# Performance work log

Hardware: AMD Instinct MI355X
Metric: run time of the kernel (lower is better)

The kernel has to match this reference:

```python
import jax, jax.numpy as jnp
import numpy as np

B, S, D = 2, 1024, 1024
H, HD = 16, 64          # n_heads, head_dim (H*HD == D)
E, FF = 8, 2816         # num_experts, moe hidden_dim
TOP_K = 2               # hard-coded torch.topk(scores, 2)
EPS = 1e-5


def rmsnorm(x, w):
    return x * jax.lax.rsqrt(jnp.mean(x * x, axis=-1, keepdims=True) + EPS) * w


def apply_rope(x, cos, sin):
    # x: [B,S,H,HD]; cos/sin: [S,HD//2] -> interleaved rotary (llama style)
    xr, xi = x[..., 0::2], x[..., 1::2]
    c = cos[None, :, None, :]
    s = sin[None, :, None, :]
    out_r = xr * c - xi * s
    out_i = xr * s + xi * c
    return jnp.stack([out_r, out_i], axis=-1).reshape(x.shape)


def setup_inputs() -> dict:
    key = jax.random.key(0)
    ks = jax.random.split(key, 10)
    sc = 0.02
    pos = jnp.arange(S, dtype=jnp.float32)
    inv = 1.0 / (10000.0 ** (jnp.arange(0, HD, 2, dtype=jnp.float32) / HD))
    ang = pos[:, None] * inv[None, :]                       # [S, HD//2]
    return {
        "x": jax.random.normal(ks[0], (B, S, D), jnp.float32),
        "freqs_cos": jnp.cos(ang),
        "freqs_sin": jnp.sin(ang),
        "attn_norm_w": jnp.ones((D,), jnp.float32),
        "wq": jax.random.normal(ks[1], (D, D), jnp.float32) * sc,
        "wk": jax.random.normal(ks[2], (D, D), jnp.float32) * sc,
        "wv": jax.random.normal(ks[3], (D, D), jnp.float32) * sc,
        "wo": jax.random.normal(ks[4], (D, D), jnp.float32) * sc,
        "ffn_norm_w": jnp.ones((D,), jnp.float32),
        "gate_w": jax.random.normal(ks[5], (E, D), jnp.float32) * sc,
        "w1": jax.random.normal(ks[6], (E, FF, D), jnp.float32) * sc,
        "w2": jax.random.normal(ks[7], (E, FF, D), jnp.float32) * sc,
        "w3": jax.random.normal(ks[8], (E, FF, D), jnp.float32) * sc,
    }


def reference(x, freqs_cos, freqs_sin, attn_norm_w, wq, wk, wv, wo,
              ffn_norm_w, gate_w, w1, w2, w3):
    b, s, d = x.shape

    # ---- pre-norm attention + residual ----
    xn = rmsnorm(x, attn_norm_w)
    q = (xn @ wq.T).reshape(b, s, H, HD)
    k = (xn @ wk.T).reshape(b, s, H, HD)
    v = (xn @ wv.T).reshape(b, s, H, HD)
    q = apply_rope(q, freqs_cos, freqs_sin)
    k = apply_rope(k, freqs_cos, freqs_sin)
    scores = jnp.einsum("bqhd,bkhd->bhqk", q, k) / jnp.sqrt(jnp.float32(HD))
    causal = jnp.tril(jnp.ones((s, s), bool))
    scores = jnp.where(causal[None, None], scores, jnp.finfo(scores.dtype).min)
    attn = jax.nn.softmax(scores, axis=-1)
    o = jnp.einsum("bhqk,bkhd->bqhd", attn, v).reshape(b, s, d) @ wo.T
    h = x + o

    # ---- top-2 MoE FFN (math identical to gather-per-token einsums) ----
    t = rmsnorm(h, ffn_norm_w).reshape(-1, d)               # [T, D]
    T = t.shape[0]
    gate = t @ gate_w.T                                     # [T, E]
    expert_weights, expert_idx = jax.lax.top_k(gate, TOP_K)
    expert_weights = jax.nn.softmax(expert_weights, axis=-1)  # [T, 2]

    x1 = jax.nn.silu(jnp.einsum("td,efd->tef", t, w1))      # [T, E, FF]
    x3 = jnp.einsum("td,efd->tef", t, w3)                   # [T, E, FF]
    ta = jnp.arange(T)[:, None]
    g = x1[ta, expert_idx] * x3[ta, expert_idx]             # [T, 2, FF]
    gw = g * expert_weights[..., None]                      # fold routing weights
    h_full = jnp.zeros((T, E, FF), t.dtype).at[ta, expert_idx].add(gw)
    moe = jnp.einsum("tef,efd->td", h_full, w2)             # [T, D]

    return h + moe.reshape(b, s, d)
```

## Files before the change

kernel.cpp:

```cpp
#include <hip/hip_runtime.h>

#define DI __device__ __forceinline__

typedef __attribute__((ext_vector_type(8))) short short8;
typedef __attribute__((ext_vector_type(4))) float f32x4;

#define DM   1024
#define TT   2048
#define SEQ  1024
#define NHD  16
#define HDD  64
#define NE   8
#define FF   2816

DI ushort f2bf(float f){
  union { float f; unsigned u; } c; c.f = f;
  unsigned u = c.u;
  u += 0x7fffu + ((u >> 16) & 1u);
  return (ushort)(u >> 16);
}
DI float bf2f(ushort b){
  union { unsigned u; float f; } c; c.u = ((unsigned)b) << 16;
  return c.f;
}
DI unsigned pk2(float a, float b){ return (unsigned)f2bf(a) | ((unsigned)f2bf(b) << 16); }
DI uint2 mku2(unsigned a, unsigned b){ uint2 r; r.x = a; r.y = b; return r; }

DI f32x4 MFMA(short8 a, short8 b, f32x4 c){
  return __builtin_amdgcn_mfma_f32_16x16x32_bf16(a, b, c, 0, 0, 0);
}

DI void gload16(const void* g, void* l){
  __builtin_amdgcn_global_load_lds(
      (const __attribute__((address_space(1))) unsigned*)g,
      (__attribute__((address_space(3))) unsigned*)l, 16, 0, 0);
}

#define LDSWZB(row, p) (((row) * 128) + ((((p) ^ ((row) & 7))) * 16))

__global__ __launch_bounds__(256) void k_rmsnorm(const float* __restrict__ x,
                                                 const float* __restrict__ w,
                                                 ushort* __restrict__ xh,
                                                 ushort* __restrict__ xl)
{
  int row = blockIdx.x, tid = threadIdx.x;
  float4 v = ((const float4*)(x + (size_t)row * DM))[tid];
  float ss = v.x*v.x + v.y*v.y + v.z*v.z + v.w*v.w;
#pragma unroll
  for (int m = 32; m >= 1; m >>= 1) ss += __shfl_xor(ss, m);
  __shared__ float sh[4];
  if ((tid & 63) == 0) sh[tid >> 6] = ss;
  __syncthreads();
  ss = sh[0] + sh[1] + sh[2] + sh[3];
  float rstd = 1.0f / sqrtf(ss * (1.0f / DM) + 1e-5f);
  float4 wv = ((const float4*)w)[tid];
  float o0 = v.x * rstd * wv.x, o1 = v.y * rstd * wv.y;
  float o2 = v.z * rstd * wv.z, o3 = v.w * rstd * wv.w;
  ushort h0 = f2bf(o0), h1 = f2bf(o1), h2 = f2bf(o2), h3 = f2bf(o3);
  ((uint2*)(xh + (size_t)row * DM))[tid] =
      mku2((unsigned)h0 | ((unsigned)h1 << 16), (unsigned)h2 | ((unsigned)h3 << 16));
  ((uint2*)(xl + (size_t)row * DM))[tid] =
      mku2(pk2(o0 - bf2f(h0), o1 - bf2f(h1)), pk2(o2 - bf2f(h2), o3 - bf2f(h3)));
}

__global__ __launch_bounds__(256) void k_wsplit(
    const float* __restrict__ wq, const float* __restrict__ wk,
    const float* __restrict__ wv, const float* __restrict__ wo,
    ushort* __restrict__ qh, ushort* __restrict__ ql,
    ushort* __restrict__ kh, ushort* __restrict__ kl,
    ushort* __restrict__ vh, ushort* __restrict__ vl,
    ushort* __restrict__ oh, ushort* __restrict__ ol)
{
  int y = blockIdx.y;
  const float* W = y == 0 ? wq : (y == 1 ? wk : (y == 2 ? wv : wo));
  ushort* H = y == 0 ? qh : (y == 1 ? kh : (y == 2 ? vh : oh));
  ushort* L = y == 0 ? ql : (y == 1 ? kl : (y == 2 ? vl : ol));
  int i = blockIdx.x * 256 + threadIdx.x;
  float4 v = ((const float4*)W)[i];
  ushort h0 = f2bf(v.x), h1 = f2bf(v.y), h2 = f2bf(v.z), h3 = f2bf(v.w);
  ((uint2*)H)[i] = mku2((unsigned)h0 | ((unsigned)h1 << 16),
                        (unsigned)h2 | ((unsigned)h3 << 16));
  ((uint2*)L)[i] = mku2(pk2(v.x - bf2f(h0), v.y - bf2f(h1)),
                        pk2(v.z - bf2f(h2), v.w - bf2f(h3)));
}

__global__ __launch_bounds__(256) void k_cw13(const float* __restrict__ w1,
                                              const float* __restrict__ w3,
                                              ushort* __restrict__ w1b,
                                              ushort* __restrict__ w3b)
{
  const float* src = blockIdx.y ? w3 : w1;
  ushort* dst = blockIdx.y ? w3b : w1b;
  const size_t N4 = (size_t)NE * FF * DM / 4;
  for (size_t i = (size_t)blockIdx.x * 256 + threadIdx.x; i < N4;
       i += (size_t)gridDim.x * 256) {
    float4 v = ((const float4*)src)[i];
    ((uint2*)dst)[i] = mku2(pk2(v.x, v.y), pk2(v.z, v.w));
  }
}

__global__ __launch_bounds__(256, 2) void k_gemm_qkv(
    const ushort* __restrict__ xh, const ushort* __restrict__ xl,
    const ushort* __restrict__ wqh, const ushort* __restrict__ wql,
    const ushort* __restrict__ wkh, const ushort* __restrict__ wkl,
    const ushort* __restrict__ wvh, const ushort* __restrict__ wvl,
    float* __restrict__ qf, float* __restrict__ kf,
    ushort* __restrict__ vh, ushort* __restrict__ vl)
{
  __shared__ __align__(16) char lds[65536];
  char* Ah = lds;          char* Al = lds + 16384;
  char* Bh = lds + 32768;  char* Bl = lds + 49152;
  int bn = blockIdx.x, bm = blockIdx.y;
  int which = bn >> 3, bnn = bn & 7;
  const ushort* WH = which == 0 ? wqh : (which == 1 ? wkh : wvh);
  const ushort* WL = which == 0 ? wql : (which == 1 ? wkl : wvl);
  int tid = threadIdx.x, lane = tid & 63, w = tid >> 6, wr = w >> 1, wc = w & 1;
  int r0 = lane >> 3, pp = lane & 7;
  size_t asrc[4], bsrc[4]; int cdst[4];
#pragma unroll
  for (int i = 0; i < 4; i++) {
    int c = w * 4 + i;
    int row = c * 8 + r0;
    asrc[i] = (size_t)(bm * 128 + row) * DM + (pp ^ r0) * 8;
    bsrc[i] = (size_t)(bnn * 128 + row) * DM + (pp ^ r0) * 8;
    cdst[i] = c * 1024;
  }
  f32x4 acc[4][4] = {};
  for (int kb = 0; kb < DM; kb += 64) {
    __syncthreads();
#pragma unroll
    for (int i = 0; i < 4; i++) {
      gload16(xh + asrc[i] + kb, Ah + cdst[i]);
      gload16(xl + asrc[i] + kb, Al + cdst[i]);
      gload16(WH + bsrc[i] + kb, Bh + cdst[i]);
      gload16(WL + bsrc[i] + kb, Bl + cdst[i]);
    }
    __syncthreads();
#pragma unroll
    for (int kk = 0; kk < 2; kk++) {
      int j = kk * 4 + (lane >> 4);
      short8 ar[4], al[4];
#pragma unroll
      for (int mi = 0; mi < 4; mi++) {
        int row = wr * 64 + mi * 16 + (lane & 15);
        ar[mi] = *(const short8*)(Ah + LDSWZB(row, j));
        al[mi] = *(const short8*)(Al + LDSWZB(row, j));
      }
#pragma unroll
      for (int ni = 0; ni < 4; ni++) {
        int n = wc * 64 + ni * 16 + (lane & 15);
        short8 b_h = *(const short8*)(Bh + LDSWZB(n, j));
        short8 b_l = *(const short8*)(Bl + LDSWZB(n, j));
#pragma unroll
        for (int mi = 0; mi < 4; mi++) {
          acc[mi][ni] = MFMA(ar[mi], b_h, acc[mi][ni]);
          acc[mi][ni] = MFMA(al[mi], b_h, acc[mi][ni]);
          acc[mi][ni] = MFMA(ar[mi], b_l, acc[mi][ni]);
        }
      }
    }
  }
#pragma unroll
  for (int mi = 0; mi < 4; mi++)
#pragma unroll
    for (int ni = 0; ni < 4; ni++)
#pragma unroll
      for (int r = 0; r < 4; r++) {
        int rg = bm*128 + wr*64 + mi*16 + (lane >> 4)*4 + r;
        int cg = bnn*128 + wc*64 + ni*16 + (lane & 15);
        float v = acc[mi][ni][r];
        if (which == 0)      qf[(size_t)rg * DM + cg] = v;
        else if (which == 1) kf[(size_t)rg * DM + cg] = v;
        else {
          int b = rg >> 10, s = rg & 1023, hh = cg >> 6, hd = cg & 63;
          size_t o = ((size_t)((b*NHD + hh)*HDD + hd)) * SEQ + s;
          ushort hv = f2bf(v);
          vh[o] = hv; vl[o] = f2bf(v - bf2f(hv));
        }
      }
}

__global__ __launch_bounds__(256) void k_rope(
    const float* __restrict__ qf, const float* __restrict__ kf,
    const float* __restrict__ fc, const float* __restrict__ fs,
    ushort* __restrict__ qh, ushort* __restrict__ ql,
    ushort* __restrict__ kh, ushort* __restrict__ kl)
{
  int t = blockIdx.x, tid = threadIdx.x;
  int b = t >> 10, s = t & 1023;
#pragma unroll
  for (int i = 0; i < 2; i++) {
    int p = tid + i*256;
    int hh = p >> 5, pi = p & 31;
    float c = fc[s*32 + pi], sn = fs[s*32 + pi];
    size_t o = ((size_t)(b*NHD + hh) * SEQ + s) * HDD + pi*2;
    {
      float2 v = *(const float2*)(qf + (size_t)t * DM + hh*HDD + pi*2);
      float r0 = v.x*c - v.y*sn, r1 = v.x*sn + v.y*c;
      ushort a0 = f2bf(r0), a1 = f2bf(r1);
      *(unsigned*)(qh + o) = (unsigned)a0 | ((unsigned)a1 << 16);
      *(unsigned*)(ql + o) = pk2(r0 - bf2f(a0), r1 - bf2f(a1));
    }
    {
      float2 v = *(const float2*)(kf + (size_t)t * DM + hh*HDD + pi*2);
      float r0 = v.x*c - v.y*sn, r1 = v.x*sn + v.y*c;
      ushort a0 = f2bf(r0), a1 = f2bf(r1);
      *(unsigned*)(kh + o) = (unsigned)a0 | ((unsigned)a1 << 16);
      *(unsigned*)(kl + o) = pk2(r0 - bf2f(a0), r1 - bf2f(a1));
    }
  }
}

__global__ __launch_bounds__(256) void k_attn(
    const ushort* __restrict__ qh_, const ushort* __restrict__ ql_,
    const ushort* __restrict__ kh_, const ushort* __restrict__ kl_,
    const ushort* __restrict__ vh_, const ushort* __restrict__ vl_,
    ushort* __restrict__ oh_, ushort* __restrict__ ol_)
{
  __shared__ __align__(16) ushort Kh[64*64], Kl[64*64], Vh[64*64], Vl[64*64];
  __shared__ __align__(16) ushort Ph[4*16*64], Pl[4*16*64];
  int qt = blockIdx.x, bh = blockIdx.y;
  int tid = threadIdx.x, lane = tid & 63, w = tid >> 6;
  short8 qfh[2], qfl[2];
  int qrow = qt*64 + w*16 + (lane & 15);
#pragma unroll
  for (int ks = 0; ks < 2; ks++) {
    size_t g = ((size_t)bh * SEQ + qrow) * HDD + ks*32 + (lane >> 4)*8;
    qfh[ks] = *(const short8*)(qh_ + g);
    qfl[ks] = *(const short8*)(ql_ + g);
  }
  f32x4 oacc[4] = {};
  float mrun[4], lrun[4];
#pragma unroll
  for (int r = 0; r < 4; r++) { mrun[r] = -1e30f; lrun[r] = 0.0f; }

  for (int kt = 0; kt <= qt; kt++) {
    __syncthreads();
#pragma unroll
    for (int i = 0; i < 2; i++) {
      int c = tid + i*256, row = c >> 3, sl = c & 7;
      int d = row*64 + ((sl + row) & 7) * 8;
      size_t gk = ((size_t)bh * SEQ + kt*64 + row) * HDD + sl*8;
      *(uint4*)&Kh[d] = *(const uint4*)(kh_ + gk);
      *(uint4*)&Kl[d] = *(const uint4*)(kl_ + gk);
      size_t gv = ((size_t)bh * HDD + row) * SEQ + kt*64 + sl*8;
      *(uint4*)&Vh[d] = *(const uint4*)(vh_ + gv);
      *(uint4*)&Vl[d] = *(const uint4*)(vl_ + gv);
    }
    __syncthreads();
    f32x4 sa[4] = {};
#pragma unroll
    for (int j = 0; j < 4; j++) {
#pragma unroll
      for (int ks = 0; ks < 2; ks++) {
        int kr = j*16 + (lane & 15);
        int d = kr*64 + (((ks*4 + (lane >> 4)) + kr) & 7) * 8;
        short8 b_h = *(const short8*)&Kh[d];
        short8 b_l = *(const short8*)&Kl[d];
        sa[j] = MFMA(qfh[ks], b_h, sa[j]);
        sa[j] = MFMA(qfl[ks], b_h, sa[j]);
        sa[j] = MFMA(qfh[ks], b_l, sa[j]);
      }
    }
    float sv[4][4];
#pragma unroll
    for (int j = 0; j < 4; j++)
#pragma unroll
      for (int r = 0; r < 4; r++) {
        float xx = sa[j][r] * 0.125f;
        if (kt == qt) {
          int kv = j*16 + (lane & 15), qi = w*16 + (lane >> 4)*4 + r;
          if (kv > qi) xx = -1e30f;
        }
        sv[j][r] = xx;
      }
#pragma unroll
    for (int r = 0; r < 4; r++) {
      float mx = fmaxf(fmaxf(sv[0][r], sv[1][r]), fmaxf(sv[2][r], sv[3][r]));
#pragma unroll
      for (int m = 8; m >= 1; m >>= 1) mx = fmaxf(mx, __shfl_xor(mx, m));
      float mn = fmaxf(mrun[r], mx);
      float alp = __expf(mrun[r] - mn);
      mrun[r] = mn;
      float rs = 0.0f;
#pragma unroll
      for (int j = 0; j < 4; j++) { float pv = __expf(sv[j][r] - mn); sv[j][r] = pv; rs += pv; }
#pragma unroll
      for (int m = 8; m >= 1; m >>= 1) rs += __shfl_xor(rs, m);
      lrun[r] = lrun[r] * alp + rs;
#pragma unroll
      for (int hf = 0; hf < 4; hf++) oacc[hf][r] *= alp;
    }
#pragma unroll
    for (int j = 0; j < 4; j++)
#pragma unroll
      for (int r = 0; r < 4; r++) {
        int row = (lane >> 4)*4 + r, col = j*16 + (lane & 15);
        int d = w*1024 + row*64 + (((col >> 3) ^ (row & 7)) * 8) + (col & 7);
        ushort hv = f2bf(sv[j][r]);
        Ph[d] = hv; Pl[d] = f2bf(sv[j][r] - bf2f(hv));
      }
#pragma unroll
    for (int hf = 0; hf < 4; hf++) {
#pragma unroll
      for (int ks = 0; ks < 2; ks++) {
        int prow = lane & 15;
        int pg = ((ks*4 + (lane >> 4)) ^ (prow & 7)) * 8;
        short8 pfh = *(const short8*)&Ph[w*1024 + prow*64 + pg];
        short8 pfl = *(const short8*)&Pl[w*1024 + prow*64 + pg];
        int vrow = hf*16 + (lane & 15);
        int vd = vrow*64 + (((ks*4 + (lane >> 4)) + vrow) & 7) * 8;
        short8 vfh = *(const short8*)&Vh[vd];
        short8 vfl = *(const short8*)&Vl[vd];
        oacc[hf] = MFMA(pfh, vfh, oacc[hf]);
        oacc[hf] = MFMA(pfl, vfh, oacc[hf]);
        oacc[hf] = MFMA(pfh, vfl, oacc[hf]);
      }
    }
  }
  int b = bh >> 4, h = bh & 15;
#pragma unroll
  for (int r = 0; r < 4; r++) {
    float li = 1.0f / lrun[r];
    int srow = qt*64 + w*16 + (lane >> 4)*4 + r;
#pragma unroll
    for (int hf = 0; hf < 4; hf++) {
      float v = oacc[hf][r] * li;
      size_t o = ((size_t)(b*SEQ + srow)) * DM + h*HDD + hf*16 + (lane & 15);
      ushort hv = f2bf(v);
      oh_[o] = hv; ol_[o] = f2bf(v - bf2f(hv));
    }
  }
}

__global__ __launch_bounds__(256, 2) void k_gemm_wo(
    const ushort* __restrict__ oh, const ushort* __restrict__ ol,
    const ushort* __restrict__ woh, const ushort* __restrict__ wol,
    const float* __restrict__ x, float* __restrict__ hb)
{
  __shared__ __align__(16) char lds[49152];
  char* Ah = lds;          char* Al = lds + 8192;
  char* Bh = lds + 16384;  char* Bl = lds + 32768;
  int bnn = blockIdx.x, bm = blockIdx.y;
  int tid = threadIdx.x, lane = tid & 63, w = tid >> 6;
  int r0 = lane >> 3, pp = lane & 7;
  size_t asrc[2]; int adst[2];
#pragma unroll
  for (int i = 0; i < 2; i++) {
    int c = w * 2 + i;
    int row = c * 8 + r0;
    asrc[i] = (size_t)(bm * 64 + row) * DM + (pp ^ r0) * 8;
    adst[i] = c * 1024;
  }
  size_t bsrc[4]; int bdst[4];
#pragma unroll
  for (int i = 0; i < 4; i++) {
    int c = w * 4 + i;
    int row = c * 8 + r0;
    bsrc[i] = (size_t)(bnn * 128 + row) * DM + (pp ^ r0) * 8;
    bdst[i] = c * 1024;
  }
  f32x4 acc[4][2] = {};
  for (int kb = 0; kb < DM; kb += 64) {
    __syncthreads();
#pragma unroll
    for (int i = 0; i < 2; i++) {
      gload16(oh + asrc[i] + kb, Ah + adst[i]);
      gload16(ol + asrc[i] + kb, Al + adst[i]);
    }
#pragma unroll
    for (int i = 0; i < 4; i++) {
      gload16(woh + bsrc[i] + kb, Bh + bdst[i]);
      gload16(wol + bsrc[i] + kb, Bl + bdst[i]);
    }
    __syncthreads();
#pragma unroll
    for (int kk = 0; kk < 2; kk++) {
      int j = kk * 4 + (lane >> 4);
      short8 ar[4], al[4];
#pragma unroll
      for (int mi = 0; mi < 4; mi++) {
        int row = mi * 16 + (lane & 15);
        ar[mi] = *(const short8*)(Ah + LDSWZB(row, j));
        al[mi] = *(const short8*)(Al + LDSWZB(row, j));
      }
#pragma unroll
      for (int ni = 0; ni < 2; ni++) {
        int n = w * 32 + ni * 16 + (lane & 15);
        short8 b_h = *(const short8*)(Bh + LDSWZB(n, j));
        short8 b_l = *(const short8*)(Bl + LDSWZB(n, j));
#pragma unroll
        for (int mi = 0; mi < 4; mi++) {
          acc[mi][ni] = MFMA(ar[mi], b_h, acc[mi][ni]);
          acc[mi][ni] = MFMA(al[mi], b_h, acc[mi][ni]);
          acc[mi][ni] = MFMA(ar[mi], b_l, acc[mi][ni]);
        }
      }
    }
  }
#pragma unroll
  for (int mi = 0; mi < 4; mi++)
#pragma unroll
    for (int ni = 0; ni < 2; ni++)
#pragma unroll
      for (int r = 0; r < 4; r++) {
        int rg = bm*64 + mi*16 + (lane >> 4)*4 + r;
        int cg = bnn*128 + w*32 + ni*16 + (lane & 15);
        hb[(size_t)rg * DM + cg] = x[(size_t)rg * DM + cg] + acc[mi][ni][r];
      }
}

__global__ __launch_bounds__(256) void k_gate(
    const float* __restrict__ hb, const float* __restrict__ fw, const float* __restrict__ gwt,
    ushort* __restrict__ tb, int* __restrict__ idx, float* __restrict__ ew, int* __restrict__ cnt)
{
  int t = blockIdx.x, tid = threadIdx.x;
  float4 v = ((const float4*)(hb + (size_t)t * DM))[tid];
  float ss = v.x*v.x + v.y*v.y + v.z*v.z + v.w*v.w;
#pragma unroll
  for (int m = 32; m >= 1; m >>= 1) ss += __shfl_xor(ss, m);
  __shared__ float sh[4];
  if ((tid & 63) == 0) sh[tid >> 6] = ss;
  __syncthreads();
  ss = sh[0] + sh[1] + sh[2] + sh[3];
  float rstd = 1.0f / sqrtf(ss * (1.0f / DM) + 1e-5f);
  float4 wv = ((const float4*)fw)[tid];
  float tv0 = v.x*rstd*wv.x, tv1 = v.y*rstd*wv.y, tv2 = v.z*rstd*wv.z, tv3 = v.w*rstd*wv.w;
  ((uint2*)(tb + (size_t)t * DM))[tid] = mku2(pk2(tv0, tv1), pk2(tv2, tv3));
  float ge[8];
#pragma unroll
  for (int e = 0; e < 8; e++) {
    float4 gv = ((const float4*)(gwt + (size_t)e * DM))[tid];
    float s = tv0*gv.x + tv1*gv.y + tv2*gv.z + tv3*gv.w;
#pragma unroll
    for (int m = 32; m >= 1; m >>= 1) s += __shfl_xor(s, m);
    ge[e] = s;
  }
  __shared__ float gsh[4][8];
  if ((tid & 63) == 0) {
#pragma unroll
    for (int e = 0; e < 8; e++) gsh[tid >> 6][e] = ge[e];
  }
  __syncthreads();
  if (tid == 0) {
    float lg[8];
#pragma unroll
    for (int e = 0; e < 8; e++) lg[e] = gsh[0][e] + gsh[1][e] + gsh[2][e] + gsh[3][e];
    int i0 = 0;
    for (int e = 1; e < 8; e++) if (lg[e] > lg[i0]) i0 = e;
    int i1 = (i0 == 0) ? 1 : 0;
    for (int e = 0; e < 8; e++) if (e != i0 && lg[e] > lg[i1]) i1 = e;
    float ex = __expf(lg[i1] - lg[i0]);
    idx[2*t] = i0; idx[2*t+1] = i1;
    ew[2*t] = 1.0f / (1.0f + ex); ew[2*t+1] = ex / (1.0f + ex);
    atomicAdd(&cnt[i0], 1); atomicAdd(&cnt[i1], 1);
  }
}

__global__ void k_offsets(const int* __restrict__ cnt, int* __restrict__ off,
                          int* __restrict__ fil, int* __restrict__ tmap)
{
  if (threadIdx.x == 0 && blockIdx.x == 0) {
    int a = 0, nt = 0;
    for (int e = 0; e < 8; e++) {
      off[e] = a; a += cnt[e]; fil[e] = 0;
      int m = (cnt[e] + 127) >> 7;
      for (int j = 0; j < m; j++) { tmap[1 + nt] = (e << 8) | j; nt++; }
    }
    tmap[0] = nt;
  }
}

__global__ __launch_bounds__(256) void k_scatter(
    const int* __restrict__ idx, const int* __restrict__ off,
    int* __restrict__ fil, int* __restrict__ ent, int* __restrict__ pos)
{
  int t = blockIdx.x * 256 + threadIdx.x;
  if (t < TT) {
#pragma unroll
    for (int k = 0; k < 2; k++) {
      int e = idx[2*t + k];
      int p = atomicAdd(&fil[e], 1);
      int g = off[e] + p;
      ent[g] = 2*t + k;
      pos[2*t + k] = g;
    }
  }
}

__global__ __launch_bounds__(256) void k_tw2(const float* __restrict__ w2, ushort* __restrict__ w2t)
{
  int dt = blockIdx.x, ft = blockIdx.y, e = blockIdx.z;
  __shared__ ushort lt[64*72];
  int tid = threadIdx.x;
#pragma unroll
  for (int i = 0; i < 4; i++) {
    int c = tid + i*256;
    int r = c >> 4, q = c & 15;
    float4 v = *(const float4*)(w2 + ((size_t)e*FF + ft*64 + r) * DM + dt*64 + q*4);
    lt[(q*4+0)*72 + r] = f2bf(v.x);
    lt[(q*4+1)*72 + r] = f2bf(v.y);
    lt[(q*4+2)*72 + r] = f2bf(v.z);
    lt[(q*4+3)*72 + r] = f2bf(v.w);
  }
  __syncthreads();
#pragma unroll
  for (int i = 0; i < 2; i++) {
    int c = tid + i*256;
    int d = c >> 3, fq = c & 7;
    *(uint4*)(w2t + ((size_t)e*DM + dt*64 + d) * FF + ft*64 + fq*8) = *(const uint4*)&lt[d*72 + fq*8];
  }
}

__global__ __launch_bounds__(256, 4) void k_moe13(
    const ushort* __restrict__ tb, const ushort* __restrict__ w1b, const ushort* __restrict__ w3b,
    const int* __restrict__ ent, const float* __restrict__ ew,
    const int* __restrict__ cnt, const int* __restrict__ off, const int* __restrict__ tmap,
    ushort* __restrict__ gb)
{
  int y = blockIdx.y;
  if (y >= tmap[0]) return;
  int tm = tmap[1 + y];
  int e = tm >> 8, mt = tm & 255;
  int nt = blockIdx.x;
  int cn = cnt[e], oe = off[e];
  __shared__ __align__(16) char lds[32768];
  char* Ab = lds;
  char* B1 = lds + 16384;
  char* B3 = lds + 24576;
  int tid = threadIdx.x, lane = tid & 63, w = tid >> 6;
  int wr = w >> 1, wc = w & 1;
  int r0 = lane >> 3, pp = lane & 7;

  const ushort* abase = tb + (pp ^ r0) * 8;
  unsigned aoff[4];
#pragma unroll
  for (int i = 0; i < 4; i++) {
    int c = w * 4 + i;
    int r = c * 8 + r0;
    int g = oe + mt * 128 + r; if (g > 2*TT - 1) g = 2*TT - 1;
    aoff[i] = (unsigned)((ent[g] >> 1) * DM);
  }
  size_t bofs[2];
#pragma unroll
  for (int i = 0; i < 2; i++) {
    int c = 2 * w + i;
    bofs[i] = ((size_t)e * FF + nt * 64 + c * 8 + r0) * DM + (pp ^ r0) * 8;
  }

  f32x4 acc1[4][2] = {}, acc3[4][2] = {};

  for (int kb = 0; kb < DM; kb += 64) {
    __syncthreads();
#pragma unroll
    for (int i = 0; i < 4; i++)
      gload16(abase + aoff[i] + kb, Ab + (w * 4 + i) * 1024);
#pragma unroll
    for (int i = 0; i < 2; i++) {
      gload16(w1b + bofs[i] + kb, B1 + (2 * w + i) * 1024);
      gload16(w3b + bofs[i] + kb, B3 + (2 * w + i) * 1024);
    }
    __syncthreads();
#pragma unroll
    for (int kk = 0; kk < 2; kk++) {
      int j = kk * 4 + (lane >> 4);
      short8 af[4];
#pragma unroll
      for (int mi = 0; mi < 4; mi++) {
        int row = wr * 64 + mi * 16 + (lane & 15);
        af[mi] = *(const short8*)(Ab + LDSWZB(row, j));
      }
#pragma unroll
      for (int ni = 0; ni < 2; ni++) {
        int n = wc * 32 + ni * 16 + (lane & 15);
        short8 b1f = *(const short8*)(B1 + LDSWZB(n, j));
        short8 b3f = *(const short8*)(B3 + LDSWZB(n, j));
#pragma unroll
        for (int mi = 0; mi < 4; mi++) {
          acc1[mi][ni] = MFMA(af[mi], b1f, acc1[mi][ni]);
          acc3[mi][ni] = MFMA(af[mi], b3f, acc3[mi][ni]);
        }
      }
    }
  }
#pragma unroll
  for (int mi = 0; mi < 4; mi++)
#pragma unroll
    for (int ni = 0; ni < 2; ni++)
#pragma unroll
      for (int r = 0; r < 4; r++) {
        int grow = mt * 128 + wr * 64 + mi * 16 + (lane >> 4) * 4 + r;
        if (grow < cn) {
          int g = oe + grow;
          float gwv = ew[ent[g]];
          int f = nt * 64 + wc * 32 + ni * 16 + (lane & 15);
          float x1 = acc1[mi][ni][r], x3 = acc3[mi][ni][r];
          float sg = x1 / (1.0f + __expf(-x1));
          gb[(size_t)g * FF + f] = f2bf(sg * x3 * gwv);
        }
      }
}

__global__ __launch_bounds__(256, 4) void k_moe2(
    const ushort* __restrict__ gb, const ushort* __restrict__ w2t,
    const int* __restrict__ cnt, const int* __restrict__ off, const int* __restrict__ tmap,
    float* __restrict__ mr)
{
  int y = blockIdx.y;
  if (y >= tmap[0]) return;
  int tm = tmap[1 + y];
  int e = tm >> 8, mt = tm & 255;
  int nt = blockIdx.x;
  int cn = cnt[e], oe = off[e];
  __shared__ __align__(16) char lds[24576];
  char* Ab = lds; char* Bb = lds + 16384;
  int tid = threadIdx.x, lane = tid & 63, w = tid >> 6;
  int r0 = lane >> 3, pp = lane & 7;

  const ushort* abase = gb + (pp ^ r0) * 8;
  unsigned aoff[4];
#pragma unroll
  for (int i = 0; i < 4; i++) {
    int c = w * 4 + i;
    int r = c * 8 + r0;
    int g = oe + mt * 128 + r; if (g > 2*TT - 1) g = 2*TT - 1;
    aoff[i] = (unsigned)(g * FF);
  }
  size_t bofs[2];
#pragma unroll
  for (int i = 0; i < 2; i++) {
    int c = 2 * w + i;
    bofs[i] = ((size_t)e * DM + nt * 64 + c * 8 + r0) * FF + (pp ^ r0) * 8;
  }

  f32x4 acc[4][1] = {};
  f32x4 a2[2][4] = {};
  (void)acc;
  for (int kb = 0; kb < FF; kb += 64) {
    __syncthreads();
#pragma unroll
    for (int i = 0; i < 4; i++)
      gload16(abase + aoff[i] + kb, Ab + (w * 4 + i) * 1024);
#pragma unroll
    for (int i = 0; i < 2; i++)
      gload16(w2t + bofs[i] + kb, Bb + (2 * w + i) * 1024);
    __syncthreads();
#pragma unroll
    for (int kk = 0; kk < 2; kk++) {
      int j = kk * 4 + (lane >> 4);
      short8 af[2], bf[4];
#pragma unroll
      for (int mi = 0; mi < 2; mi++) {
        int row = w * 32 + mi * 16 + (lane & 15);
        af[mi] = *(const short8*)(Ab + LDSWZB(row, j));
      }
#pragma unroll
      for (int ni = 0; ni < 4; ni++) {
        int n = ni * 16 + (lane & 15);
        bf[ni] = *(const short8*)(Bb + LDSWZB(n, j));
      }
#pragma unroll
      for (int ni = 0; ni < 4; ni++)
#pragma unroll
        for (int mi = 0; mi < 2; mi++)
          a2[mi][ni] = MFMA(af[mi], bf[ni], a2[mi][ni]);
    }
  }
#pragma unroll
  for (int mi = 0; mi < 2; mi++)
#pragma unroll
    for (int ni = 0; ni < 4; ni++)
#pragma unroll
      for (int r = 0; r < 4; r++) {
        int grow = mt * 128 + w * 32 + mi * 16 + (lane >> 4) * 4 + r;
        if (grow < cn) {
          int cg = nt * 64 + ni * 16 + (lane & 15);
          mr[(size_t)(oe + grow) * DM + cg] = a2[mi][ni][r];
        }
      }
}

__global__ __launch_bounds__(256) void k_final(
    const float* __restrict__ hb, const float* __restrict__ mr,
    const int* __restrict__ pos, float* __restrict__ out)
{
  int t = blockIdx.x, tid = threadIdx.x;
  int g0 = pos[2*t], g1 = pos[2*t+1];
  float4 a  = ((const float4*)(hb + (size_t)t * DM))[tid];
  float4 m0 = ((const float4*)(mr + (size_t)g0 * DM))[tid];
  float4 m1 = ((const float4*)(mr + (size_t)g1 * DM))[tid];
  float4 o;
  o.x = a.x + m0.x + m1.x; o.y = a.y + m0.y + m1.y;
  o.z = a.z + m0.z + m1.z; o.w = a.w + m0.w + m1.w;
  ((float4*)(out + (size_t)t * DM))[tid] = o;
}

extern "C" void kernel_launch(void* const* d_in, const int* in_sizes, int n_in,
                              void* d_out, int out_size, void* d_ws, size_t ws_size,
                              hipStream_t stream)
{
  const float* x   = (const float*)d_in[0];
  const float* fc  = (const float*)d_in[1];
  const float* fs  = (const float*)d_in[2];
  const float* anw = (const float*)d_in[3];
  const float* wq  = (const float*)d_in[4];
  const float* wk  = (const float*)d_in[5];
  const float* wv  = (const float*)d_in[6];
  const float* wo  = (const float*)d_in[7];
  const float* fnw = (const float*)d_in[8];
  const float* gwm = (const float*)d_in[9];
  const float* w1  = (const float*)d_in[10];
  const float* w2  = (const float*)d_in[11];
  const float* w3  = (const float*)d_in[12];
  float* out = (float*)d_out;

  char* p = (char*)d_ws;
  auto alloc = [&](size_t n) { char* r = p; p += (n + 255) & ~(size_t)255; return r; };
  ushort* xnh = (ushort*)alloc((size_t)TT*DM*2);
  ushort* xnl = (ushort*)alloc((size_t)TT*DM*2);
  float*  qf  = (float*) alloc((size_t)TT*DM*4);
  float*  kf  = (float*) alloc((size_t)TT*DM*4);
  ushort* qh  = (ushort*)alloc((size_t)TT*DM*2);
  ushort* ql  = (ushort*)alloc((size_t)TT*DM*2);
  ushort* kh  = (ushort*)alloc((size_t)TT*DM*2);
  ushort* kl  = (ushort*)alloc((size_t)TT*DM*2);
  ushort* vh  = (ushort*)alloc((size_t)TT*DM*2);
  ushort* vl  = (ushort*)alloc((size_t)TT*DM*2);
  ushort* oh  = (ushort*)alloc((size_t)TT*DM*2);
  ushort* ol  = (ushort*)alloc((size_t)TT*DM*2);
  float*  hb  = (float*) alloc((size_t)TT*DM*4);
  ushort* tb  = (ushort*)alloc((size_t)TT*DM*2);
  ushort* w2t = (ushort*)alloc((size_t)NE*FF*DM*2);
  ushort* gb  = (ushort*)alloc((size_t)2*TT*FF*2);
  float*  mr  = (float*) alloc((size_t)2*TT*DM*4);
  int*    idx = (int*)   alloc((size_t)2*TT*4);
  float*  ew  = (float*) alloc((size_t)2*TT*4);
  int*    ent = (int*)   alloc((size_t)2*TT*4);
  int*    pos = (int*)   alloc((size_t)2*TT*4);
  int*    cnt = (int*)   alloc(32);
  int*    off = (int*)   alloc(32);
  int*    fil = (int*)   alloc(32);
  int*    tmap= (int*)   alloc(256);

  ushort* wsp = (ushort*)mr;
  const size_t WN = (size_t)DM * DM;
  ushort* wqh = wsp;        ushort* wql = wsp + WN;
  ushort* wkh = wsp + 2*WN; ushort* wkl = wsp + 3*WN;
  ushort* wvh = wsp + 4*WN; ushort* wvl = wsp + 5*WN;
  ushort* woh = wsp + 6*WN; ushort* wol = wsp + 7*WN;

  ushort* w1b = (ushort*)d_ws;
  ushort* w3b = (ushort*)alloc((size_t)NE*FF*DM*2);

  hipMemsetAsync(cnt, 0, 32, stream);
  k_rmsnorm<<<TT, 256, 0, stream>>>(x, anw, xnh, xnl);
  k_wsplit<<<dim3(1024, 4), 256, 0, stream>>>(wq, wk, wv, wo,
      wqh, wql, wkh, wkl, wvh, wvl, woh, wol);
  k_tw2<<<dim3(16, 44, 8), 256, 0, stream>>>(w2, w2t);
  k_gemm_qkv<<<dim3(24, 16), 256, 0, stream>>>(xnh, xnl,
      wqh, wql, wkh, wkl, wvh, wvl, qf, kf, vh, vl);
  k_rope<<<TT, 256, 0, stream>>>(qf, kf, fc, fs, qh, ql, kh, kl);
  k_attn<<<dim3(16, 32), 256, 0, stream>>>(qh, ql, kh, kl, vh, vl, oh, ol);
  k_gemm_wo<<<dim3(8, 32), 256, 0, stream>>>(oh, ol, woh, wol, x, hb);
  k_gate<<<TT, 256, 0, stream>>>(hb, fnw, gwm, tb, idx, ew, cnt);
  k_offsets<<<1, 64, 0, stream>>>(cnt, off, fil, tmap);
  k_scatter<<<8, 256, 0, stream>>>(idx, off, fil, ent, pos);
  k_cw13<<<dim3(2048, 2), 256, 0, stream>>>(w1, w3, w1b, w3b);
  k_moe13<<<dim3(44, 48), 256, 0, stream>>>(tb, w1b, w3b, ent, ew, cnt, off, tmap, gb);
  k_moe2<<<dim3(16, 48), 256, 0, stream>>>(gb, w2t, cnt, off, tmap, mr);
  k_final<<<TT, 256, 0, stream>>>(hb, mr, pos, out);
  (void)in_sizes; (void)n_in; (void)out_size; (void)ws_size;
}
```

Baseline: 458.5 us.

## Fuse fp32-to-bf16 conversion of w1/w3 into MoE up-projection GEMM

Drops the separate kernel that converted the full w1 and w3 expert weights to bf16. The k_moe13 GEMM now loads fp32 weight tiles into registers one k-step ahead, packs them to bf16 and stores them into swizzled LDS, with manual waitcnt and barriers so the next tile's load overlaps the current MFMA work. This removes a full write and re-read of the converted weights. In exchange each block reads fp32 weights, which is twice the bytes, and several token tiles per expert re-read them, so it also uses more registers (occupancy hint lowered from 4 to 3).

```diff
diff --git a/kernel.cpp b/kernel.cpp
--- a/kernel.cpp
+++ b/kernel.cpp
@@ -37,6 +37,11 @@
 }
 
 #define LDSWZB(row, p) (((row) * 128) + ((((p) ^ ((row) & 7))) * 16))
+
+#define VMCNT(N) asm volatile("s_waitcnt vmcnt(" #N ")" ::: "memory")
+#define LGKM0()  asm volatile("s_waitcnt lgkmcnt(0)" ::: "memory")
+#define SBAR()   __builtin_amdgcn_s_barrier()
+#define SCHED0() __builtin_amdgcn_sched_barrier(0)
 
 __global__ __launch_bounds__(256) void k_rmsnorm(const float* __restrict__ x,
                                                  const float* __restrict__ w,
@@ -84,21 +89,6 @@
                         pk2(v.z - bf2f(h2), v.w - bf2f(h3)));
 }
 
-__global__ __launch_bounds__(256) void k_cw13(const float* __restrict__ w1,
-                                              const float* __restrict__ w3,
-                                              ushort* __restrict__ w1b,
-                                              ushort* __restrict__ w3b)
-{
-  const float* src = blockIdx.y ? w3 : w1;
-  ushort* dst = blockIdx.y ? w3b : w1b;
-  const size_t N4 = (size_t)NE * FF * DM / 4;
-  for (size_t i = (size_t)blockIdx.x * 256 + threadIdx.x; i < N4;
-       i += (size_t)gridDim.x * 256) {
-    float4 v = ((const float4*)src)[i];
-    ((uint2*)dst)[i] = mku2(pk2(v.x, v.y), pk2(v.z, v.w));
-  }
-}
-
 __global__ __launch_bounds__(256, 2) void k_gemm_qkv(
     const ushort* __restrict__ xh, const ushort* __restrict__ xl,
     const ushort* __restrict__ wqh, const ushort* __restrict__ wql,
@@ -512,8 +502,8 @@
   }
 }
 
-__global__ __launch_bounds__(256, 4) void k_moe13(
-    const ushort* __restrict__ tb, const ushort* __restrict__ w1b, const ushort* __restrict__ w3b,
+__global__ __launch_bounds__(256, 3) void k_moe13(
+    const ushort* __restrict__ tb, const float* __restrict__ w1, const float* __restrict__ w3,
     const int* __restrict__ ent, const float* __restrict__ ew,
     const int* __restrict__ cnt, const int* __restrict__ off, const int* __restrict__ tmap,
     ushort* __restrict__ gb)
@@ -541,26 +531,51 @@
     int g = oe + mt * 128 + r; if (g > 2*TT - 1) g = 2*TT - 1;
     aoff[i] = (unsigned)((ent[g] >> 1) * DM);
   }
-  size_t bofs[2];
-#pragma unroll
-  for (int i = 0; i < 2; i++) {
-    int c = 2 * w + i;
-    bofs[i] = ((size_t)e * FF + nt * 64 + c * 8 + r0) * DM + (pp ^ r0) * 8;
-  }
+  int brow = tid >> 2, cq = tid & 3;
+  const float* b1p = w1 + ((size_t)e * FF + nt * 64 + brow) * DM + cq * 16;
+  const float* b3p = w3 + ((size_t)e * FF + nt * 64 + brow) * DM + cq * 16;
+  int bd0 = LDSWZB(brow, 2 * cq);
+  int bd1 = LDSWZB(brow, 2 * cq + 1);
 
   f32x4 acc1[4][2] = {}, acc3[4][2] = {};
-
-  for (int kb = 0; kb < DM; kb += 64) {
-    __syncthreads();
+  float4 r1[4], r3[4];
+#pragma unroll
+  for (int i2 = 0; i2 < 4; i2++) {
+    r1[i2] = *(const float4*)(b1p + i2 * 4);
+    r3[i2] = *(const float4*)(b3p + i2 * 4);
+  }
+
+  for (int t = 0; t < 16; t++) {
+    int kb = t * 64;
+    SBAR();
 #pragma unroll
     for (int i = 0; i < 4; i++)
       gload16(abase + aoff[i] + kb, Ab + (w * 4 + i) * 1024);
-#pragma unroll
-    for (int i = 0; i < 2; i++) {
-      gload16(w1b + bofs[i] + kb, B1 + (2 * w + i) * 1024);
-      gload16(w3b + bofs[i] + kb, B3 + (2 * w + i) * 1024);
-    }
-    __syncthreads();
+    SCHED0();
+    {
+      uint4 u;
+      u.x = pk2(r1[0].x, r1[0].y); u.y = pk2(r1[0].z, r1[0].w);
+      u.z = pk2(r1[1].x, r1[1].y); u.w = pk2(r1[1].z, r1[1].w);
+      *(uint4*)(B1 + bd0) = u;
+      u.x = pk2(r1[2].x, r1[2].y); u.y = pk2(r1[2].z, r1[2].w);
+      u.z = pk2(r1[3].x, r1[3].y); u.w = pk2(r1[3].z, r1[3].w);
+      *(uint4*)(B1 + bd1) = u;
+      u.x = pk2(r3[0].x, r3[0].y); u.y = pk2(r3[0].z, r3[0].w);
+      u.z = pk2(r3[1].x, r3[1].y); u.w = pk2(r3[1].z, r3[1].w);
+      *(uint4*)(B3 + bd0) = u;
+      u.x = pk2(r3[2].x, r3[2].y); u.y = pk2(r3[2].z, r3[2].w);
+      u.z = pk2(r3[3].x, r3[3].y); u.w = pk2(r3[3].z, r3[3].w);
+      *(uint4*)(B3 + bd1) = u;
+    }
+    int kb2 = ((t + 1) & 15) * 64;
+#pragma unroll
+    for (int i2 = 0; i2 < 4; i2++) {
+      r1[i2] = *(const float4*)(b1p + kb2 + i2 * 4);
+      r3[i2] = *(const float4*)(b3p + kb2 + i2 * 4);
+    }
+    VMCNT(8);
+    LGKM0();
+    SBAR(); SCHED0();
 #pragma unroll
     for (int kk = 0; kk < 2; kk++) {
       int j = kk * 4 + (lane >> 4);
@@ -633,9 +648,7 @@
     bofs[i] = ((size_t)e * DM + nt * 64 + c * 8 + r0) * FF + (pp ^ r0) * 8;
   }
 
-  f32x4 acc[4][1] = {};
   f32x4 a2[2][4] = {};
-  (void)acc;
   for (int kb = 0; kb < FF; kb += 64) {
     __syncthreads();
 #pragma unroll
@@ -749,9 +762,6 @@
   ushort* wvh = wsp + 4*WN; ushort* wvl = wsp + 5*WN;
   ushort* woh = wsp + 6*WN; ushort* wol = wsp + 7*WN;
 
-  ushort* w1b = (ushort*)d_ws;
-  ushort* w3b = (ushort*)alloc((size_t)NE*FF*DM*2);
-
   hipMemsetAsync(cnt, 0, 32, stream);
   k_rmsnorm<<<TT, 256, 0, stream>>>(x, anw, xnh, xnl);
   k_wsplit<<<dim3(1024, 4), 256, 0, stream>>>(wq, wk, wv, wo,
@@ -765,8 +775,7 @@
   k_gate<<<TT, 256, 0, stream>>>(hb, fnw, gwm, tb, idx, ew, cnt);
   k_offsets<<<1, 64, 0, stream>>>(cnt, off, fil, tmap);
   k_scatter<<<8, 256, 0, stream>>>(idx, off, fil, ent, pos);
-  k_cw13<<<dim3(2048, 2), 256, 0, stream>>>(w1, w3, w1b, w3b);
-  k_moe13<<<dim3(44, 48), 256, 0, stream>>>(tb, w1b, w3b, ent, ew, cnt, off, tmap, gb);
+  k_moe13<<<dim3(44, 48), 256, 0, stream>>>(tb, w1, w3, ent, ew, cnt, off, tmap, gb);
   k_moe2<<<dim3(16, 48), 256, 0, stream>>>(gb, w2t, cnt, off, tmap, mr);
   k_final<<<TT, 256, 0, stream>>>(hb, mr, pos, out);
   (void)in_sizes; (void)n_in; (void)out_size; (void)ws_size;
```

New measurement: 470.6 us. 1.03x slower.
